# Kernel optimization log

Hardware: AMD Instinct MI355X
Metric: run time of the kernel (lower is better)

Reference implementation:

```python
import jax, jax.numpy as jnp
import numpy as np

MICRO_BATCHES = 4
NUM_EXPERTS = 8  # world_size=1 -> num_local_experts = 8
EPS = 1e-5


def setup_inputs() -> dict:
    key = jax.random.key(0)
    ks = jax.random.split(key, 8)
    B, S, D = 8, 2048, 1024
    E, F = NUM_EXPERTS, 4 * D
    x = jax.random.normal(ks[0], (B, S, D), dtype=jnp.float32)
    gamma = jnp.ones((D,), jnp.float32)
    beta = jnp.zeros((D,), jnp.float32)
    gate_w = jax.random.normal(ks[1], (E, D), jnp.float32) * (1.0 / np.sqrt(D))
    w1 = jax.random.normal(ks[2], (E, D, F), jnp.float32) * (1.0 / np.sqrt(D))
    b1 = jnp.zeros((E, F), jnp.float32)
    w2 = jax.random.normal(ks[3], (E, F, D), jnp.float32) * (1.0 / np.sqrt(F))
    b2 = jnp.zeros((E, D), jnp.float32)
    return {"x": x, "gamma": gamma, "beta": beta, "gate_w": gate_w,
            "w1": w1, "b1": b1, "w2": w2, "b2": b2}


def reference(x, gamma, beta, gate_w, w1, b1, w2, b2):
    B, S, D = x.shape
    E = w1.shape[0]
    # micro-batch chunking along batch dim (chunk(MICRO_BATCHES, dim=0))
    xf = x.reshape(MICRO_BATCHES, -1, D)            # [MB, T, D], T = B/MB * S
    T = xf.shape[1]
    # residual (gated_input) is the pre-LN flat input
    # moe_norm: LayerNorm over last dim, biased variance, eps=1e-5
    mu = jnp.mean(xf, axis=-1, keepdims=True)
    var = jnp.mean(jnp.square(xf - mu), axis=-1, keepdims=True)
    xn = (xf - mu) * jax.lax.rsqrt(var + EPS) * gamma + beta  # [MB, T, D]
    # gate logits + topk are computed in the source but discarded
    _logits = jnp.einsum('mtd,ed->mte', xn, gate_w)
    _ = jax.lax.top_k(_logits, 2)
    # dispatch/combine are identity for world_size=1; tokens split round-robin
    # into num_local_experts contiguous chunks per micro-batch
    tpe = T // E
    xe = xn.reshape(MICRO_BATCHES, E, tpe, D)       # [MB, E, tpe, D]
    h = jax.nn.gelu(jnp.einsum('metd,edf->metf', xe, w1) + b1[None, :, None, :],
                    approximate=False)
    y = jnp.einsum('metf,efd->metd', h, w2) + b2[None, :, None, :]
    out = xf + y.reshape(MICRO_BATCHES, T, D)       # residual add
    return out.reshape(B, S, D)
```

## Files before the change

### kernel.cpp

```cpp
#include <hip/hip_runtime.h>
#include <stdint.h>
#include <math.h>

typedef unsigned short ushort_t;
typedef __attribute__((ext_vector_type(8))) short bf16x8;
typedef __attribute__((ext_vector_type(4))) float f32x4;

#define SLOT 32768
#define EPI_STRIDE 1032

__device__ __forceinline__ ushort_t f2bf(float f) {
  union { float f; unsigned u; } cv; cv.f = f;
  unsigned r = cv.u + 0x7fffu + ((cv.u >> 16) & 1u);
  return (ushort_t)(r >> 16);
}

__device__ __forceinline__ void gl_lds16(const void* g, void* l) {
  typedef __attribute__((address_space(1))) const char gchar;
  typedef __attribute__((address_space(3))) char lchar;
  __builtin_amdgcn_global_load_lds((gchar*)g, (lchar*)l, 16, 0, 0);
}

__device__ __forceinline__ f32x4 MFMA(bf16x8 a, bf16x8 b, f32x4 c) {
  return __builtin_amdgcn_mfma_f32_16x16x32_bf16(a, b, c, 0, 0, 0);
}

__global__ __launch_bounds__(256) void ln_kernel(const float* __restrict__ x,
                                                 const float* __restrict__ gamma,
                                                 const float* __restrict__ beta,
                                                 ushort_t* __restrict__ xn) {
  const int row = blockIdx.x;
  const int t = threadIdx.x;
  const float4 v = ((const float4*)(x + (size_t)row * 1024))[t];
  float s  = v.x + v.y + v.z + v.w;
  float ss = v.x * v.x + v.y * v.y + v.z * v.z + v.w * v.w;
#pragma unroll
  for (int o = 32; o >= 1; o >>= 1) {
    s  += __shfl_xor(s, o);
    ss += __shfl_xor(ss, o);
  }
  __shared__ float red[10];
  const int wave = t >> 6, lane = t & 63;
  if (lane == 0) { red[wave] = s; red[4 + wave] = ss; }
  __syncthreads();
  if (t == 0) {
    float S  = red[0] + red[1] + red[2] + red[3];
    float SS = red[4] + red[5] + red[6] + red[7];
    float mu  = S * (1.0f / 1024.0f);
    float var = SS * (1.0f / 1024.0f) - mu * mu;
    red[8] = mu;
    red[9] = rsqrtf(var + 1e-5f);
  }
  __syncthreads();
  const float mu = red[8], rs = red[9];
  const float4 g = ((const float4*)gamma)[t];
  const float4 b = ((const float4*)beta)[t];
  ushort4 o;
  o.x = f2bf((v.x - mu) * rs * g.x + b.x);
  o.y = f2bf((v.y - mu) * rs * g.y + b.y);
  o.z = f2bf((v.z - mu) * rs * g.z + b.z);
  o.w = f2bf((v.w - mu) * rs * g.w + b.w);
  ((ushort4*)(xn + (size_t)row * 1024))[t] = o;
}

__global__ __launch_bounds__(256) void transpose_cast(const float* __restrict__ in,
                                                      ushort_t* __restrict__ out,
                                                      int R, int C) {
  __shared__ float tile[32][33];
  const int e = blockIdx.z;
  const float* src = in + (size_t)e * R * C;
  ushort_t* dst = out + (size_t)e * R * C;
  const int c0 = blockIdx.x * 32, r0 = blockIdx.y * 32;
  const int tx = threadIdx.x, ty = threadIdx.y;
#pragma unroll
  for (int j = 0; j < 32; j += 8)
    tile[ty + j][tx] = src[(size_t)(r0 + ty + j) * C + c0 + tx];
  __syncthreads();
#pragma unroll
  for (int j = 0; j < 32; j += 8)
    dst[(size_t)(c0 + ty + j) * R + r0 + tx] = f2bf(tile[tx][ty + j]);
}


__device__ __forceinline__ void stage_half(const ushort_t* gsrc, int lda,
                                           char* half_base, int kt, int tid) {
  const int rr = tid >> 2;
  const int gs = (tid & 3) ^ ((tid >> 3) & 3);
  gl_lds16(gsrc + (size_t)rr * lda + kt + gs * 8, half_base + (tid >> 6) * 1024);
}

template <int BASE>
__device__ __forceinline__ void mfma16(const bf16x8 (&a)[4], const bf16x8 (&b)[4],
                                       f32x4 (&acc)[8][4]) {
  __builtin_amdgcn_s_setprio(1);
#pragma unroll
  for (int mi = 0; mi < 4; mi++)
#pragma unroll
    for (int ni = 0; ni < 4; ni++)
      acc[BASE + mi][ni] = MFMA(a[mi], b[ni], acc[BASE + mi][ni]);
  __builtin_amdgcn_s_setprio(0);
}

template <int VM, bool STG, bool LAST>
__device__ __forceinline__ void tile_body(char* smem, int T,
                                          const ushort_t* gA, const ushort_t* gB,
                                          int lda, int a_off, int b_off, int tid,
                                          bf16x8 (&bA0)[4], bf16x8 (&bA1)[4],
                                          bf16x8 (&bBc)[4], bf16x8 (&bBn)[4],
                                          f32x4 (&acc)[8][4]) {
  const char* slot = smem + (T & 3) * SLOT;
  char* nstg = smem + ((T + 3) & 3) * SLOT;
  const int kt3 = (T + 3) * 32;
#pragma unroll
  for (int mi = 0; mi < 4; mi++) bA1[mi] = *(const bf16x8*)(slot + a_off + (mi + 4) * 1024);
  if (STG) {
    stage_half(gA, lda, nstg, kt3, tid);
    stage_half(gA + (size_t)128 * lda, lda, nstg + 8192, kt3, tid);
  }
  __builtin_amdgcn_sched_barrier(0);
  __builtin_amdgcn_s_barrier();
  __builtin_amdgcn_sched_barrier(0);
  mfma16<0>(bA0, bBc, acc);
  __builtin_amdgcn_s_barrier();
  if (VM == 6)      asm volatile("s_waitcnt vmcnt(6)" ::: "memory");
  else if (VM == 4) asm volatile("s_waitcnt vmcnt(4)" ::: "memory");
  else if (VM == 0) asm volatile("s_waitcnt vmcnt(0)" ::: "memory");
  __builtin_amdgcn_s_barrier();
  if (!LAST) {
    const char* nslot = smem + ((T + 1) & 3) * SLOT;
#pragma unroll
    for (int ni = 0; ni < 4; ni++) bBn[ni] = *(const bf16x8*)(nslot + b_off + ni * 1024);
#pragma unroll
    for (int mi = 0; mi < 4; mi++) bA0[mi] = *(const bf16x8*)(nslot + a_off + mi * 1024);
    if (STG) {
      stage_half(gB, lda, nstg + 16384, kt3, tid);
      stage_half(gB + (size_t)128 * lda, lda, nstg + 24576, kt3, tid);
    }
  }
  __builtin_amdgcn_sched_barrier(0);
  mfma16<4>(bA1, bBc, acc);
  __builtin_amdgcn_s_barrier();
}

template <int EPI, int LDA, int LDC, int KTOT>
__global__ __launch_bounds__(512, 2) void gemm256(const ushort_t* __restrict__ A,
                                                  const ushort_t* __restrict__ Bw,
                                                  const float* __restrict__ bias,
                                                  const float* __restrict__ resid,
                                                  ushort_t* __restrict__ Hout,
                                                  float* __restrict__ Fout) {
  extern __shared__ char smem[];
  const int tid = threadIdx.x;
  const int wave = tid >> 6, lane = tid & 63;

  const int bid = blockIdx.x;
  const int c = bid & 7, l = bid >> 3;
  const int tm = c * 8 + (l & 7);
  const int tn = l >> 3;
  const int row0 = tm * 256;
  const int col0 = tn * 256;
  const int e = (row0 >> 9) & 7;

  const ushort_t* gA = A + (size_t)row0 * LDA;
  const ushort_t* gB = Bw + ((size_t)e * LDC + col0) * LDA;

  const int NT = KTOT / 32;

  const int wm = wave >> 2, wn = wave & 3;
  const int l15 = lane & 15, g = lane >> 4;
  const int sw = ((g ^ ((lane >> 1) & 3)) << 4);
  const int a_off = wm * 8192 + l15 * 64 + sw;
  const int b_off = 16384 + (wn >> 1) * 8192 + (wn & 1) * 4096 + l15 * 64 + sw;

  f32x4 acc[8][4] = {};
  bf16x8 bA0[4], bA1[4], bB0[4], bB1[4];

#pragma unroll
  for (int T = 0; T < 3; ++T) {
    char* s = smem + T * SLOT;
    stage_half(gA, LDA, s, T * 32, tid);
    stage_half(gA + (size_t)128 * LDA, LDA, s + 8192, T * 32, tid);
    stage_half(gB, LDA, s + 16384, T * 32, tid);
    stage_half(gB + (size_t)128 * LDA, LDA, s + 24576, T * 32, tid);
  }
  asm volatile("s_waitcnt vmcnt(8)" ::: "memory");
  __builtin_amdgcn_s_barrier();
#pragma unroll
  for (int ni = 0; ni < 4; ni++) bB0[ni] = *(const bf16x8*)(smem + b_off + ni * 1024);
#pragma unroll
  for (int mi = 0; mi < 4; mi++) bA0[mi] = *(const bf16x8*)(smem + a_off + mi * 1024);

  for (int T = 0; T < NT - 4; T += 2) {
    tile_body<6, true, false>(smem, T,     gA, gB, LDA, a_off, b_off, tid, bA0, bA1, bB0, bB1, acc);
    tile_body<6, true, false>(smem, T + 1, gA, gB, LDA, a_off, b_off, tid, bA0, bA1, bB1, bB0, acc);
  }
  tile_body<6, true,  false>(smem, NT - 4, gA, gB, LDA, a_off, b_off, tid, bA0, bA1, bB0, bB1, acc);
  tile_body<4, false, false>(smem, NT - 3, gA, gB, LDA, a_off, b_off, tid, bA0, bA1, bB1, bB0, acc);
  tile_body<0, false, false>(smem, NT - 2, gA, gB, LDA, a_off, b_off, tid, bA0, bA1, bB0, bB1, acc);
  tile_body<-1, false, true>(smem, NT - 1, gA, gB, LDA, a_off, b_off, tid, bA0, bA1, bB1, bB0, acc);

  __syncthreads();

  float bv[4];
#pragma unroll
  for (int ni = 0; ni < 4; ni++)
    bv[ni] = bias[e * LDC + col0 + wn * 64 + ni * 16 + l15];

#pragma unroll
  for (int r = 0; r < 4; ++r) {
#pragma unroll
    for (int mh = 0; mh < 2; ++mh) {
      const int mi = 2 * r + mh;
      const int lrow = wm * 32 + mh * 16 + g * 4;
#pragma unroll
      for (int ni = 0; ni < 4; ++ni) {
        const int colb = (wn * 64 + ni * 16 + l15) * 4;
#pragma unroll
        for (int rr = 0; rr < 4; ++rr) {
          float v = acc[mi][ni][rr] + bv[ni];
          if (EPI == 0) {
            float v2 = v * v;
            float cc = fmaf(0.044715f, v2, 1.0f);
            float u  = exp2f(-2.3022078f * v * cc);
            v = __fdividef(v, 1.0f + u);
          }
          *(float*)(smem + (size_t)(lrow + rr) * EPI_STRIDE + colb) = v;
        }
      }
    }
    __syncthreads();
#pragma unroll
    for (int i = 0; i < 8; ++i) {
      const int chunk = i * 512 + tid;
      const int lr = chunk >> 6;
      const int cb = (chunk & 63) * 16;
      const float4 v4 = *(const float4*)(smem + (size_t)lr * EPI_STRIDE + cb);
      const int grow = row0 + (lr < 32 ? r * 32 + lr : 128 + r * 32 + (lr - 32));
      const int gcol = col0 + (chunk & 63) * 4;
      if (EPI == 0) {
        ushort4 o;
        o.x = f2bf(v4.x); o.y = f2bf(v4.y); o.z = f2bf(v4.z); o.w = f2bf(v4.w);
        *(ushort4*)(&Hout[(size_t)grow * LDC + gcol]) = o;
      } else {
        const float4 rs = *(const float4*)(&resid[(size_t)grow * LDC + gcol]);
        float4 o;
        o.x = v4.x + rs.x; o.y = v4.y + rs.y; o.z = v4.z + rs.z; o.w = v4.w + rs.w;
        *(float4*)(&Fout[(size_t)grow * LDC + gcol]) = o;
      }
    }
    __syncthreads();
  }
}

extern "C" void kernel_launch(void* const* d_in, const int* in_sizes, int n_in,
                              void* d_out, int out_size, void* d_ws, size_t ws_size,
                              hipStream_t stream) {
  const float* x     = (const float*)d_in[0];
  const float* gamma = (const float*)d_in[1];
  const float* beta  = (const float*)d_in[2];
  const float* w1    = (const float*)d_in[4];
  const float* b1    = (const float*)d_in[5];
  const float* w2    = (const float*)d_in[6];
  const float* b2    = (const float*)d_in[7];
  float* out = (float*)d_out;

  char* ws = (char*)d_ws;
  ushort_t* xn  = (ushort_t*)ws;
  ushort_t* w1t = (ushort_t*)(ws + 33554432);
  ushort_t* w2t = (ushort_t*)(ws + 33554432 + 67108864);
  ushort_t* h   = (ushort_t*)(ws + 33554432 + 2 * 67108864);

  hipFuncSetAttribute(reinterpret_cast<const void*>(&gemm256<0, 1024, 4096, 1024>),
                      hipFuncAttributeMaxDynamicSharedMemorySize, 131072);
  hipFuncSetAttribute(reinterpret_cast<const void*>(&gemm256<1, 4096, 1024, 4096>),
                      hipFuncAttributeMaxDynamicSharedMemorySize, 131072);

  ln_kernel<<<16384, 256, 0, stream>>>(x, gamma, beta, xn);
  transpose_cast<<<dim3(128, 32, 8), dim3(32, 8), 0, stream>>>(w1, w1t, 1024, 4096);
  transpose_cast<<<dim3(32, 128, 8), dim3(32, 8), 0, stream>>>(w2, w2t, 4096, 1024);

  gemm256<0, 1024, 4096, 1024><<<dim3(1024), 512, 131072, stream>>>(xn, w1t, b1, nullptr, h, nullptr);
  gemm256<1, 4096, 1024, 4096><<<dim3(256), 512, 131072, stream>>>(h, w2t, b2, x, nullptr, out);
}
```

Before: 424.0 us.

## Replace pipelined 256x256 GEMM with simple single-buffered 128x128 GEMM

Replaces the 512-thread, 256x256-tile GEMM, which had a 4-slot global-to-LDS prefetch pipeline and explicit vmcnt waits, with a 256-thread 128x128-tile kernel. The new kernel loads one K-step, synchronises, runs its MFMAs and synchronises again. This removes the large dynamic shared memory footprint and quadruples the grid size, so more blocks can be resident per CU. The cost is no load/compute overlap inside a block and half the data reuse per tile, so it leans on occupancy to hide latency.

```diff
diff --git a/kernel.cpp b/kernel.cpp
--- a/kernel.cpp
+++ b/kernel.cpp
@@ -6,8 +6,7 @@
 typedef __attribute__((ext_vector_type(8))) short bf16x8;
 typedef __attribute__((ext_vector_type(4))) float f32x4;
 
-#define SLOT 32768
-#define EPI_STRIDE 1032
+#define EPI_STRIDE 528
 
 __device__ __forceinline__ ushort_t f2bf(float f) {
   union { float f; unsigned u; } cv; cv.f = f;
@@ -82,161 +81,100 @@
 }
 
 
-__device__ __forceinline__ void stage_half(const ushort_t* gsrc, int lda,
-                                           char* half_base, int kt, int tid) {
-  const int rr = tid >> 2;
-  const int gs = (tid & 3) ^ ((tid >> 3) & 3);
-  gl_lds16(gsrc + (size_t)rr * lda + kt + gs * 8, half_base + (tid >> 6) * 1024);
-}
-
-template <int BASE>
-__device__ __forceinline__ void mfma16(const bf16x8 (&a)[4], const bf16x8 (&b)[4],
-                                       f32x4 (&acc)[8][4]) {
-  __builtin_amdgcn_s_setprio(1);
-#pragma unroll
-  for (int mi = 0; mi < 4; mi++)
-#pragma unroll
-    for (int ni = 0; ni < 4; ni++)
-      acc[BASE + mi][ni] = MFMA(a[mi], b[ni], acc[BASE + mi][ni]);
-  __builtin_amdgcn_s_setprio(0);
-}
-
-template <int VM, bool STG, bool LAST>
-__device__ __forceinline__ void tile_body(char* smem, int T,
-                                          const ushort_t* gA, const ushort_t* gB,
-                                          int lda, int a_off, int b_off, int tid,
-                                          bf16x8 (&bA0)[4], bf16x8 (&bA1)[4],
-                                          bf16x8 (&bBc)[4], bf16x8 (&bBn)[4],
-                                          f32x4 (&acc)[8][4]) {
-  const char* slot = smem + (T & 3) * SLOT;
-  char* nstg = smem + ((T + 3) & 3) * SLOT;
-  const int kt3 = (T + 3) * 32;
-#pragma unroll
-  for (int mi = 0; mi < 4; mi++) bA1[mi] = *(const bf16x8*)(slot + a_off + (mi + 4) * 1024);
-  if (STG) {
-    stage_half(gA, lda, nstg, kt3, tid);
-    stage_half(gA + (size_t)128 * lda, lda, nstg + 8192, kt3, tid);
-  }
-  __builtin_amdgcn_sched_barrier(0);
-  __builtin_amdgcn_s_barrier();
-  __builtin_amdgcn_sched_barrier(0);
-  mfma16<0>(bA0, bBc, acc);
-  __builtin_amdgcn_s_barrier();
-  if (VM == 6)      asm volatile("s_waitcnt vmcnt(6)" ::: "memory");
-  else if (VM == 4) asm volatile("s_waitcnt vmcnt(4)" ::: "memory");
-  else if (VM == 0) asm volatile("s_waitcnt vmcnt(0)" ::: "memory");
-  __builtin_amdgcn_s_barrier();
-  if (!LAST) {
-    const char* nslot = smem + ((T + 1) & 3) * SLOT;
-#pragma unroll
-    for (int ni = 0; ni < 4; ni++) bBn[ni] = *(const bf16x8*)(nslot + b_off + ni * 1024);
-#pragma unroll
-    for (int mi = 0; mi < 4; mi++) bA0[mi] = *(const bf16x8*)(nslot + a_off + mi * 1024);
-    if (STG) {
-      stage_half(gB, lda, nstg + 16384, kt3, tid);
-      stage_half(gB + (size_t)128 * lda, lda, nstg + 24576, kt3, tid);
-    }
-  }
-  __builtin_amdgcn_sched_barrier(0);
-  mfma16<4>(bA1, bBc, acc);
-  __builtin_amdgcn_s_barrier();
-}
-
-template <int EPI, int LDA, int LDC, int KTOT>
-__global__ __launch_bounds__(512, 2) void gemm256(const ushort_t* __restrict__ A,
-                                                  const ushort_t* __restrict__ Bw,
-                                                  const float* __restrict__ bias,
-                                                  const float* __restrict__ resid,
-                                                  ushort_t* __restrict__ Hout,
-                                                  float* __restrict__ Fout) {
-  extern __shared__ char smem[];
+template <int EPI, int LDA, int LDC, int KTOT, int LOG_NTN>
+__global__ __launch_bounds__(256) void gemm128(const ushort_t* __restrict__ A,
+                                               const ushort_t* __restrict__ Bw,
+                                               const float* __restrict__ bias,
+                                               const float* __restrict__ resid,
+                                               ushort_t* __restrict__ Hout,
+                                               float* __restrict__ Fout) {
+  __shared__ char smem[32 * EPI_STRIDE];
   const int tid = threadIdx.x;
   const int wave = tid >> 6, lane = tid & 63;
 
   const int bid = blockIdx.x;
   const int c = bid & 7, l = bid >> 3;
-  const int tm = c * 8 + (l & 7);
-  const int tn = l >> 3;
-  const int row0 = tm * 256;
-  const int col0 = tn * 256;
-  const int e = (row0 >> 9) & 7;
+  const int tm = c * 16 + (l >> LOG_NTN);
+  const int tn = l & ((1 << LOG_NTN) - 1);
+  const int row0 = tm * 128;
+  const int col0 = tn * 128;
+  const int e = (tm >> 2) & 7;
 
   const ushort_t* gA = A + (size_t)row0 * LDA;
   const ushort_t* gB = Bw + ((size_t)e * LDC + col0) * LDA;
 
-  const int NT = KTOT / 32;
-
-  const int wm = wave >> 2, wn = wave & 3;
+  const int srow = wave * 16 + (lane >> 2);
+  const int gs = ((lane & 3) ^ ((lane >> 3) & 3)) * 8;
+  char* const dA0 = smem + wave * 1024;
+  char* const dA1 = smem + 4096 + wave * 1024;
+  char* const dB0 = smem + 8192 + wave * 1024;
+  char* const dB1 = smem + 12288 + wave * 1024;
+
+  const int wr = wave >> 1, wc = wave & 1;
   const int l15 = lane & 15, g = lane >> 4;
-  const int sw = ((g ^ ((lane >> 1) & 3)) << 4);
-  const int a_off = wm * 8192 + l15 * 64 + sw;
-  const int b_off = 16384 + (wn >> 1) * 8192 + (wn & 1) * 4096 + l15 * 64 + sw;
-
-  f32x4 acc[8][4] = {};
-  bf16x8 bA0[4], bA1[4], bB0[4], bB1[4];
-
-#pragma unroll
-  for (int T = 0; T < 3; ++T) {
-    char* s = smem + T * SLOT;
-    stage_half(gA, LDA, s, T * 32, tid);
-    stage_half(gA + (size_t)128 * LDA, LDA, s + 8192, T * 32, tid);
-    stage_half(gB, LDA, s + 16384, T * 32, tid);
-    stage_half(gB + (size_t)128 * LDA, LDA, s + 24576, T * 32, tid);
-  }
-  asm volatile("s_waitcnt vmcnt(8)" ::: "memory");
-  __builtin_amdgcn_s_barrier();
-#pragma unroll
-  for (int ni = 0; ni < 4; ni++) bB0[ni] = *(const bf16x8*)(smem + b_off + ni * 1024);
-#pragma unroll
-  for (int mi = 0; mi < 4; mi++) bA0[mi] = *(const bf16x8*)(smem + a_off + mi * 1024);
-
-  for (int T = 0; T < NT - 4; T += 2) {
-    tile_body<6, true, false>(smem, T,     gA, gB, LDA, a_off, b_off, tid, bA0, bA1, bB0, bB1, acc);
-    tile_body<6, true, false>(smem, T + 1, gA, gB, LDA, a_off, b_off, tid, bA0, bA1, bB1, bB0, acc);
-  }
-  tile_body<6, true,  false>(smem, NT - 4, gA, gB, LDA, a_off, b_off, tid, bA0, bA1, bB0, bB1, acc);
-  tile_body<4, false, false>(smem, NT - 3, gA, gB, LDA, a_off, b_off, tid, bA0, bA1, bB1, bB0, acc);
-  tile_body<0, false, false>(smem, NT - 2, gA, gB, LDA, a_off, b_off, tid, bA0, bA1, bB0, bB1, acc);
-  tile_body<-1, false, true>(smem, NT - 1, gA, gB, LDA, a_off, b_off, tid, bA0, bA1, bB1, bB0, acc);
-
-  __syncthreads();
+  const int sw = ((g ^ ((l15 >> 1) & 3)) << 4);
+  const int a_off = wr * 4096 + l15 * 64 + sw;
+  const int b_off = 8192 + wc * 4096 + l15 * 64 + sw;
+
+  f32x4 acc[4][4] = {};
+
+  for (int kt = 0; kt < KTOT; kt += 32) {
+    gl_lds16(gA + (size_t)srow * LDA + kt + gs,        dA0);
+    gl_lds16(gA + (size_t)(srow + 64) * LDA + kt + gs, dA1);
+    gl_lds16(gB + (size_t)srow * LDA + kt + gs,        dB0);
+    gl_lds16(gB + (size_t)(srow + 64) * LDA + kt + gs, dB1);
+    __syncthreads();
+    bf16x8 a[4], b[4];
+#pragma unroll
+    for (int ni = 0; ni < 4; ni++) b[ni] = *(const bf16x8*)(smem + b_off + ni * 1024);
+#pragma unroll
+    for (int mi = 0; mi < 4; mi++) a[mi] = *(const bf16x8*)(smem + a_off + mi * 1024);
+#pragma unroll
+    for (int mi = 0; mi < 4; mi++)
+#pragma unroll
+      for (int ni = 0; ni < 4; ni++)
+        acc[mi][ni] = MFMA(a[mi], b[ni], acc[mi][ni]);
+    __syncthreads();
+  }
 
   float bv[4];
 #pragma unroll
   for (int ni = 0; ni < 4; ni++)
-    bv[ni] = bias[e * LDC + col0 + wn * 64 + ni * 16 + l15];
+    bv[ni] = bias[e * LDC + col0 + wc * 64 + ni * 16 + l15];
 
 #pragma unroll
   for (int r = 0; r < 4; ++r) {
-#pragma unroll
-    for (int mh = 0; mh < 2; ++mh) {
-      const int mi = 2 * r + mh;
-      const int lrow = wm * 32 + mh * 16 + g * 4;
-#pragma unroll
-      for (int ni = 0; ni < 4; ++ni) {
-        const int colb = (wn * 64 + ni * 16 + l15) * 4;
-#pragma unroll
-        for (int rr = 0; rr < 4; ++rr) {
-          float v = acc[mi][ni][rr] + bv[ni];
-          if (EPI == 0) {
-            float v2 = v * v;
-            float cc = fmaf(0.044715f, v2, 1.0f);
-            float u  = exp2f(-2.3022078f * v * cc);
-            v = __fdividef(v, 1.0f + u);
+    if (wr == (r >> 1)) {
+#pragma unroll
+      for (int mh = 0; mh < 2; ++mh) {
+        const int lrow = mh * 16 + g * 4;
+#pragma unroll
+        for (int ni = 0; ni < 4; ++ni) {
+          const int colb = (wc * 64 + ni * 16 + l15) * 4;
+          const int mi = (r & 1) * 2 + mh;
+#pragma unroll
+          for (int rr = 0; rr < 4; ++rr) {
+            float v = acc[mi][ni][rr] + bv[ni];
+            if (EPI == 0) {
+              float v2 = v * v;
+              float cc = fmaf(0.044715f, v2, 1.0f);
+              float u  = exp2f(-2.3022078f * v * cc);
+              v = __fdividef(v, 1.0f + u);
+            }
+            *(float*)(smem + (size_t)(lrow + rr) * EPI_STRIDE + colb) = v;
           }
-          *(float*)(smem + (size_t)(lrow + rr) * EPI_STRIDE + colb) = v;
         }
       }
     }
     __syncthreads();
 #pragma unroll
-    for (int i = 0; i < 8; ++i) {
-      const int chunk = i * 512 + tid;
-      const int lr = chunk >> 6;
-      const int cb = (chunk & 63) * 16;
-      const float4 v4 = *(const float4*)(smem + (size_t)lr * EPI_STRIDE + cb);
-      const int grow = row0 + (lr < 32 ? r * 32 + lr : 128 + r * 32 + (lr - 32));
-      const int gcol = col0 + (chunk & 63) * 4;
+    for (int i = 0; i < 4; ++i) {
+      const int chunk = i * 256 + tid;
+      const int lr = chunk >> 5;
+      const int c4 = chunk & 31;
+      const float4 v4 = *(const float4*)(smem + (size_t)lr * EPI_STRIDE + c4 * 16);
+      const int grow = row0 + r * 32 + lr;
+      const int gcol = col0 + c4 * 4;
       if (EPI == 0) {
         ushort4 o;
         o.x = f2bf(v4.x); o.y = f2bf(v4.y); o.z = f2bf(v4.z); o.w = f2bf(v4.w);
@@ -270,15 +208,10 @@
   ushort_t* w2t = (ushort_t*)(ws + 33554432 + 67108864);
   ushort_t* h   = (ushort_t*)(ws + 33554432 + 2 * 67108864);
 
-  hipFuncSetAttribute(reinterpret_cast<const void*>(&gemm256<0, 1024, 4096, 1024>),
-                      hipFuncAttributeMaxDynamicSharedMemorySize, 131072);
-  hipFuncSetAttribute(reinterpret_cast<const void*>(&gemm256<1, 4096, 1024, 4096>),
-                      hipFuncAttributeMaxDynamicSharedMemorySize, 131072);
-
   ln_kernel<<<16384, 256, 0, stream>>>(x, gamma, beta, xn);
   transpose_cast<<<dim3(128, 32, 8), dim3(32, 8), 0, stream>>>(w1, w1t, 1024, 4096);
   transpose_cast<<<dim3(32, 128, 8), dim3(32, 8), 0, stream>>>(w2, w2t, 4096, 1024);
 
-  gemm256<0, 1024, 4096, 1024><<<dim3(1024), 512, 131072, stream>>>(xn, w1t, b1, nullptr, h, nullptr);
-  gemm256<1, 4096, 1024, 4096><<<dim3(256), 512, 131072, stream>>>(h, w2t, b2, x, nullptr, out);
-}
+  gemm128<0, 1024, 4096, 1024, 5><<<dim3(4096), 256, 0, stream>>>(xn, w1t, b1, nullptr, h, nullptr);
+  gemm128<1, 4096, 1024, 4096, 3><<<dim3(1024), 256, 0, stream>>>(h, w2t, b2, x, nullptr, out);
+}
```

Measured after the change: 616.9 us. 1.45x slower.
